# Optimization experiments

Hardware: AMD Instinct MI355X
Metric: run time of the kernel (lower is better)

The kernel has to match this reference:

```python
import jax, jax.numpy as jnp
import numpy as np

K = 3
STRIDE = 1
PAD = 1
DIL = 1


def conv2d(x, w, b, stride, pad, dil):
    y = jax.lax.conv_general_dilated(
        x, w, (stride, stride), [(pad, pad), (pad, pad)],
        rhs_dilation=(dil, dil), dimension_numbers=("NCHW", "OIHW", "NCHW"))
    return y + b[None, :, None, None]


def bilinear_gather(img, ys, xs):
    # img: (C,H,W); ys,xs: (KK,Ho,Wo) pixel coords.
    # grid_sample(mode=bilinear, padding_mode=zeros, align_corners=True):
    # out-of-range corners contribute 0, interpolation weights unchanged.
    H, W = img.shape[-2:]
    y0 = jnp.floor(ys)
    x0 = jnp.floor(xs)
    wy1 = ys - y0
    wx1 = xs - x0
    wy0 = 1.0 - wy1
    wx0 = 1.0 - wx1

    def g(yc, xc):
        yi = yc.astype(jnp.int32)
        xi = xc.astype(jnp.int32)
        valid = (yi >= 0) & (yi < H) & (xi >= 0) & (xi < W)
        yi = jnp.clip(yi, 0, H - 1)
        xi = jnp.clip(xi, 0, W - 1)
        v = img[:, yi, xi]  # (C,KK,Ho,Wo)
        return v * valid[None].astype(img.dtype)

    return (g(y0, x0) * (wy0 * wx0)[None]
            + g(y0, x0 + 1.0) * (wy0 * wx1)[None]
            + g(y0 + 1.0, x0) * (wy1 * wx0)[None]
            + g(y0 + 1.0, x0 + 1.0) * (wy1 * wx1)[None])


def setup_inputs() -> dict:
    key = jax.random.key(0)
    ks = jax.random.split(key, 4)
    B, C_in, H, W = 8, 64, 96, 96
    C_out = 64
    x = jax.random.normal(ks[0], (B, C_in, H, W), dtype=jnp.float32)
    weight = jax.random.normal(ks[1], (C_out, C_in, K, K), dtype=jnp.float32) * 0.05
    bias = jax.random.normal(ks[2], (C_out,), dtype=jnp.float32) * 0.01
    off_w = jax.random.normal(ks[3], (2 * K * K, C_in, K, K), dtype=jnp.float32) * 0.05
    off_b = jnp.zeros((2 * K * K,), dtype=jnp.float32)
    return {"x": x, "weight": weight, "bias": bias, "off_w": off_w, "off_b": off_b}


def reference(x, weight, bias, off_w, off_b):
    B, C, H, W = x.shape
    Ho = (H + 2 * PAD - DIL * (K - 1) - 1) // STRIDE + 1
    Wo = (W + 2 * PAD - DIL * (K - 1) - 1) // STRIDE + 1

    offsets = conv2d(x, off_w, off_b, STRIDE, PAD, DIL)  # (B,2*K*K,Ho,Wo)
    off = offsets.reshape(B, K * K, 2, Ho, Wo)

    # Base sampling grid (note: original code does NOT subtract padding; kept faithful).
    by, bx = jnp.meshgrid(jnp.arange(Ho, dtype=x.dtype), jnp.arange(Wo, dtype=x.dtype), indexing="ij")
    by = by * STRIDE + (K // 2) * DIL
    bx = bx * STRIDE + (K // 2) * DIL
    ko = jnp.arange(-(K // 2), K // 2 + 1, dtype=x.dtype)
    ky, kx = jnp.meshgrid(ko, ko, indexing="ij")

    sy = by[None, None] + ky.reshape(1, -1, 1, 1) + off[:, :, 0]  # (B,KK,Ho,Wo)
    sx = bx[None, None] + kx.reshape(1, -1, 1, 1) + off[:, :, 1]

    sampled = jax.vmap(bilinear_gather)(x, sy, sx)  # (B,C,KK,Ho,Wo)

    wflat = weight.reshape(weight.shape[0], C, K * K)  # (O,C,KK)
    out = jnp.einsum("bckhw,ock->bohw", sampled, wflat)
    return out + bias[None, :, None, None]
```

## Files before the change

### kernel.cpp

```cpp
#include <hip/hip_runtime.h>
#include <hip/hip_bf16.h>

#define HH 96
#define WW 96
#define HW 9216
#define NB 8

typedef __bf16 bf16x8 __attribute__((ext_vector_type(8)));
typedef float  f32x4  __attribute__((ext_vector_type(4)));

union BF8 { uint4 u; bf16x8 v; unsigned short s[8]; };

__device__ __forceinline__ unsigned short f2bf_bits(float f) {
    unsigned u = __float_as_uint(f);
    unsigned r = u + 0x7FFFu + ((u >> 16) & 1u);
    return (unsigned short)(r >> 16);
}
__device__ __forceinline__ float bf2f(unsigned short s) {
    return __uint_as_float(((unsigned)s) << 16);
}
__device__ __forceinline__ unsigned pkbf(float a, float b) {
    union { __hip_bfloat162 h; unsigned u; } c;
    c.h = __float22bfloat162_rn(make_float2(a, b));
    return c.u;
}

__device__ __forceinline__ void bl_setup(int h, int w, int r, int s, float oy, float ox,
                                         int* a, float* wg) {
    float sy = (float)(h + r) + oy;
    float sx = (float)(w + s) + ox;
    float fy = floorf(sy), fx = floorf(sx);
    int   y0 = (int)fy, x0 = (int)fx;
    int   y1 = y0 + 1, x1 = x0 + 1;
    float wy1 = sy - fy, wx1 = sx - fx;
    float wy0 = 1.f - wy1, wx0 = 1.f - wx1;
    float m00 = (y0 >= 0 && y0 < HH && x0 >= 0 && x0 < WW) ? 1.f : 0.f;
    float m01 = (y0 >= 0 && y0 < HH && x1 >= 0 && x1 < WW) ? 1.f : 0.f;
    float m10 = (y1 >= 0 && y1 < HH && x0 >= 0 && x0 < WW) ? 1.f : 0.f;
    float m11 = (y1 >= 0 && y1 < HH && x1 >= 0 && x1 < WW) ? 1.f : 0.f;
    int cy0 = min(max(y0, 0), HH - 1), cy1 = min(max(y1, 0), HH - 1);
    int cx0 = min(max(x0, 0), WW - 1), cx1 = min(max(x1, 0), WW - 1);
    a[0] = (cy0 * WW + cx0) * 64;  a[1] = (cy0 * WW + cx1) * 64;
    a[2] = (cy1 * WW + cx0) * 64;  a[3] = (cy1 * WW + cx1) * 64;
    wg[0] = wy0 * wx0 * m00;  wg[1] = wy0 * wx1 * m01;
    wg[2] = wy1 * wx0 * m10;  wg[3] = wy1 * wx1 * m11;
}

__global__ __launch_bounds__(256) void xcvt_prep(const float* __restrict__ x,
                                                 const float* __restrict__ weight,
                                                 const float* __restrict__ off_w,
                                                 unsigned short* __restrict__ xt,
                                                 unsigned short* __restrict__ wTb,
                                                 unsigned short* __restrict__ owTb) {
    __shared__ unsigned short T[64 * 64];
    int bid   = blockIdx.x;
    int t     = threadIdx.x;
    int b     = bid & 7;
    int pbase = (bid >> 3) * 64;
    int pl    = t & 63;
    int q     = t >> 6;

    const float* xp = x + ((size_t)(b * 64 + q * 16)) * HW + pbase + pl;
    unsigned short hb[16];
#pragma unroll
    for (int i = 0; i < 16; ++i) hb[i] = f2bf_bits(xp[(size_t)i * HW]);

    uint4 w0, w1;
    w0.x = hb[0]  | (hb[1]  << 16); w0.y = hb[2]  | (hb[3]  << 16);
    w0.z = hb[4]  | (hb[5]  << 16); w0.w = hb[6]  | (hb[7]  << 16);
    w1.x = hb[8]  | (hb[9]  << 16); w1.y = hb[10] | (hb[11] << 16);
    w1.z = hb[12] | (hb[13] << 16); w1.w = hb[14] | (hb[15] << 16);
    int sw = pl & 7;
    *(uint4*)&T[pl * 64 + (((2 * q)     ^ sw) << 3)] = w0;
    *(uint4*)&T[pl * 64 + (((2 * q + 1) ^ sw) << 3)] = w1;
    __syncthreads();

    int row = t >> 2, rs = row & 7;
    uint4 a  = *(const uint4*)&T[row * 64 + ((((t & 3) * 2)     ^ rs) << 3)];
    uint4 b2 = *(const uint4*)&T[row * 64 + ((((t & 3) * 2 + 1) ^ rs) << 3)];
    unsigned short* dst = xt + ((size_t)(b * HW + pbase)) * 64 + t * 16;
    *(uint4*)dst       = a;
    *(uint4*)(dst + 8) = b2;

    if (bid < 216) {
        int i = bid * 256 + t;
        if (i < 36864) {
            int tap = i >> 12;
            int co  = (i >> 6) & 63;
            int c   = i & 63;
            wTb[i] = f2bf_bits(weight[(co * 64 + c) * 9 + tap]);
        } else {
            int f   = i - 36864;
            int j   = f / 576;
            int kk  = f - j * 576;
            int tap = kk >> 6;
            int c   = kk & 63;
            owTb[f] = (j < 18) ? f2bf_bits(off_w[(j * 64 + c) * 9 + tap]) : (unsigned short)0;
        }
    }
}

__global__ __launch_bounds__(256) void deform_all(const unsigned short* __restrict__ xt,
                                                  const unsigned short* __restrict__ wTb,
                                                  const unsigned short* __restrict__ owTb,
                                                  const float* __restrict__ bias,
                                                  const float* __restrict__ ob,
                                                  float* __restrict__ out) {
    __shared__ unsigned short S[2][32 * 64];
    __shared__ float offs[32 * 20];

    int bid   = blockIdx.x;
    int t     = threadIdx.x;
    int b     = bid & 7;
    int pbase = (bid >> 3) * 32;

    int e   = t & 7;
    int pxl = t >> 3;
    int px  = pbase + pxl;
    int h   = px / WW, w = px - h * WW;
    int sw  = pxl & 7;

    int ln = t & 15;
    int qd = (t >> 4) & 3;
    int wv = t >> 6;

    const unsigned short* xb = xt + (size_t)b * HW * 64;

    int ptA = wv & 1, jtA = wv >> 1;
    f32x4 accj = {0.f, 0.f, 0.f, 0.f};

    for (int tap = 0; tap < 9; ++tap) {
        int cur = tap & 1;
        int r = tap / 3, s = tap - r * 3;

        int  iy = h - 1 + r, ix = w - 1 + s;
        bool vd = (iy >= 0) & (iy < HH) & (ix >= 0) & (ix < WW);
        int  ad = (min(max(iy, 0), HH - 1) * WW + min(max(ix, 0), WW - 1)) * 64;
        uint4 p = *(const uint4*)(xb + ad + e * 8);
        if (!vd) p = make_uint4(0, 0, 0, 0);
        *(uint4*)&S[cur][pxl * 64 + ((e ^ sw) << 3)] = p;
        __syncthreads();

        int  row = ptA * 16 + ln, rs = row & 7;
        BF8  fa0, fa1, fb0, fb1;
        fa0.u = *(const uint4*)&S[cur][row * 64 + ((qd       ^ rs) << 3)];
        fa1.u = *(const uint4*)&S[cur][row * 64 + (((qd + 4) ^ rs) << 3)];
        const unsigned short* brow = owTb + (size_t)(jtA * 16 + ln) * 576 + tap * 64 + qd * 8;
        fb0.u = *(const uint4*)brow;
        fb1.u = *(const uint4*)(brow + 32);
        accj = __builtin_amdgcn_mfma_f32_16x16x32_bf16(fa0.v, fb0.v, accj, 0, 0, 0);
        accj = __builtin_amdgcn_mfma_f32_16x16x32_bf16(fa1.v, fb1.v, accj, 0, 0, 0);
    }

    {
        int j = jtA * 16 + ln;
        if (j < 18) {
            int   rowp = ptA * 16 + qd * 4;
            float obj  = ob[j];
#pragma unroll
            for (int rg = 0; rg < 4; ++rg) offs[(rowp + rg) * 20 + j] = accj[rg] + obj;
        }
    }
    __syncthreads();

    float oy[9], ox[9];
#pragma unroll
    for (int k = 0; k < 9; ++k) {
        float2 p = *(const float2*)&offs[pxl * 20 + 2 * k];
        oy[k] = p.x; ox[k] = p.y;
    }

    f32x4 acc[2] = {{0.f,0.f,0.f,0.f},{0.f,0.f,0.f,0.f}};

    for (int tap = 0; tap < 9; ++tap) {
        int cur = tap & 1;
        int r = tap / 3, s = tap - r * 3;

        int   a[4];
        float g[4];
        bl_setup(h, w, r, s, oy[tap], ox[tap], a, g);

        uint4 cA[4];
#pragma unroll
        for (int c = 0; c < 4; ++c) cA[c] = *(const uint4*)(xb + a[c] + e * 8);

        BF8 q0, q1, q2, q3;
        q0.u = cA[0]; q1.u = cA[1]; q2.u = cA[2]; q3.u = cA[3];
        float v[8];
#pragma unroll
        for (int i = 0; i < 8; ++i)
            v[i] = g[0] * bf2f(q0.s[i]) + g[1] * bf2f(q1.s[i])
                 + g[2] * bf2f(q2.s[i]) + g[3] * bf2f(q3.s[i]);
        uint4 sv;
        sv.x = pkbf(v[0], v[1]); sv.y = pkbf(v[2], v[3]);
        sv.z = pkbf(v[4], v[5]); sv.w = pkbf(v[6], v[7]);
        *(uint4*)&S[cur][pxl * 64 + ((e ^ sw) << 3)] = sv;
        __syncthreads();

        {
            const unsigned short* wb = wTb + (size_t)tap * 4096 + (wv * 16 + ln) * 64 + qd * 8;
            BF8 fb0, fb1;
            fb0.u = *(const uint4*)wb;
            fb1.u = *(const uint4*)(wb + 32);
#pragma unroll
            for (int pt = 0; pt < 2; ++pt) {
                int row = pt * 16 + ln, rs = row & 7;
                BF8 fa0, fa1;
                fa0.u = *(const uint4*)&S[cur][row * 64 + ((qd       ^ rs) << 3)];
                fa1.u = *(const uint4*)&S[cur][row * 64 + (((qd + 4) ^ rs) << 3)];
                acc[pt] = __builtin_amdgcn_mfma_f32_16x16x32_bf16(fa0.v, fb0.v, acc[pt], 0, 0, 0);
                acc[pt] = __builtin_amdgcn_mfma_f32_16x16x32_bf16(fa1.v, fb1.v, acc[pt], 0, 0, 0);
            }
        }
    }

    int   co = wv * 16 + ln;
    float bv = bias[co];
    float* ob2 = out + ((size_t)(b * 64 + co)) * HW + pbase + qd * 4;
#pragma unroll
    for (int pt = 0; pt < 2; ++pt) {
        float4 st;
        st.x = acc[pt].x + bv; st.y = acc[pt].y + bv;
        st.z = acc[pt].z + bv; st.w = acc[pt].w + bv;
        *(float4*)(ob2 + pt * 16) = st;
    }
}

extern "C" void kernel_launch(void* const* d_in, const int* in_sizes, int n_in,
                              void* d_out, int out_size, void* d_ws, size_t ws_size,
                              hipStream_t stream) {
    const float* x      = (const float*)d_in[0];
    const float* weight = (const float*)d_in[1];
    const float* bias   = (const float*)d_in[2];
    const float* off_w  = (const float*)d_in[3];
    const float* off_b  = (const float*)d_in[4];
    float* out = (float*)d_out;

    unsigned short* xt   = (unsigned short*)d_ws;
    unsigned short* wTb  = xt + 4718592;
    unsigned short* owTb = wTb + 36864;

    hipLaunchKernelGGL(xcvt_prep,  dim3(1152), dim3(256), 0, stream,
                       x, weight, off_w, xt, wTb, owTb);
    hipLaunchKernelGGL(deform_all, dim3(2304), dim3(256), 0, stream,
                       xt, wTb, owTb, bias, off_b, out);
}
```

Before: 136.1 us.

## Stage 3-row halo in LDS for offset conv and software-pipeline bilinear gathers

The offset-conv phase now loads a 3x34-pixel halo tile into shared memory once, then reads all 9 taps from it. This replaces a global load and barrier per tap. The deformable phase processes two taps per barrier step and issues the gathers for the next two taps before computing the current ones, to hide global latency. Launch bounds request 3 blocks per SM. The change assumes each 32-pixel block lies within one image row (96 is divisible by 32), and it raises register pressure from the prefetched gather buffers.

```diff
diff --git a/kernel.cpp b/kernel.cpp
--- a/kernel.cpp
+++ b/kernel.cpp
@@ -100,24 +100,25 @@
     }
 }
 
-__global__ __launch_bounds__(256) void deform_all(const unsigned short* __restrict__ xt,
-                                                  const unsigned short* __restrict__ wTb,
-                                                  const unsigned short* __restrict__ owTb,
-                                                  const float* __restrict__ bias,
-                                                  const float* __restrict__ ob,
-                                                  float* __restrict__ out) {
-    __shared__ unsigned short S[2][32 * 64];
+__global__ __launch_bounds__(256, 3) void deform_all(const unsigned short* __restrict__ xt,
+                                                     const unsigned short* __restrict__ wTb,
+                                                     const unsigned short* __restrict__ owTb,
+                                                     const float* __restrict__ bias,
+                                                     const float* __restrict__ ob,
+                                                     float* __restrict__ out) {
+    __shared__ unsigned short SH[2 * 2 * 32 * 64];
     __shared__ float offs[32 * 20];
 
     int bid   = blockIdx.x;
     int t     = threadIdx.x;
     int b     = bid & 7;
     int pbase = (bid >> 3) * 32;
+    int r0    = pbase / WW;
+    int c0    = pbase - r0 * WW;
 
     int e   = t & 7;
     int pxl = t >> 3;
-    int px  = pbase + pxl;
-    int h   = px / WW, w = px - h * WW;
+    int h   = r0, w = c0 + pxl;
     int sw  = pxl & 7;
 
     int ln = t & 15;
@@ -126,32 +127,36 @@
 
     const unsigned short* xb = xt + (size_t)b * HW * 64;
 
+#pragma unroll
+    for (int p = 0; p < 4; ++p) {
+        int rec = p * 32 + pxl;
+        if (rec < 102) {
+            int hr = rec / 34, hc = rec - hr * 34;
+            int gr = r0 - 1 + hr, gc = c0 - 1 + hc;
+            bool vd = (gr >= 0) & (gr < HH) & (gc >= 0) & (gc < WW);
+            uint4 v = make_uint4(0u, 0u, 0u, 0u);
+            if (vd) v = *(const uint4*)(xb + (size_t)(gr * WW + gc) * 64 + e * 8);
+            *(uint4*)&SH[rec * 64 + ((e ^ (hc & 7)) << 3)] = v;
+        }
+    }
+    __syncthreads();
+
     int ptA = wv & 1, jtA = wv >> 1;
     f32x4 accj = {0.f, 0.f, 0.f, 0.f};
-
+#pragma unroll
     for (int tap = 0; tap < 9; ++tap) {
-        int cur = tap & 1;
         int r = tap / 3, s = tap - r * 3;
-
-        int  iy = h - 1 + r, ix = w - 1 + s;
-        bool vd = (iy >= 0) & (iy < HH) & (ix >= 0) & (ix < WW);
-        int  ad = (min(max(iy, 0), HH - 1) * WW + min(max(ix, 0), WW - 1)) * 64;
-        uint4 p = *(const uint4*)(xb + ad + e * 8);
-        if (!vd) p = make_uint4(0, 0, 0, 0);
-        *(uint4*)&S[cur][pxl * 64 + ((e ^ sw) << 3)] = p;
-        __syncthreads();
-
-        int  row = ptA * 16 + ln, rs = row & 7;
-        BF8  fa0, fa1, fb0, fb1;
-        fa0.u = *(const uint4*)&S[cur][row * 64 + ((qd       ^ rs) << 3)];
-        fa1.u = *(const uint4*)&S[cur][row * 64 + (((qd + 4) ^ rs) << 3)];
+        int cH = ptA * 16 + ln + s;
+        int ba = (r * 34 + cH) * 64;
+        BF8 fa0, fa1, fb0, fb1;
+        fa0.u = *(const uint4*)&SH[ba + ((qd       ^ (cH & 7)) << 3)];
+        fa1.u = *(const uint4*)&SH[ba + (((qd + 4) ^ (cH & 7)) << 3)];
         const unsigned short* brow = owTb + (size_t)(jtA * 16 + ln) * 576 + tap * 64 + qd * 8;
         fb0.u = *(const uint4*)brow;
         fb1.u = *(const uint4*)(brow + 32);
         accj = __builtin_amdgcn_mfma_f32_16x16x32_bf16(fa0.v, fb0.v, accj, 0, 0, 0);
         accj = __builtin_amdgcn_mfma_f32_16x16x32_bf16(fa1.v, fb1.v, accj, 0, 0, 0);
     }
-
     {
         int j = jtA * 16 + ln;
         if (j < 18) {
@@ -172,46 +177,70 @@
 
     f32x4 acc[2] = {{0.f,0.f,0.f,0.f},{0.f,0.f,0.f,0.f}};
 
-    for (int tap = 0; tap < 9; ++tap) {
-        int cur = tap & 1;
+    uint4 cc[2][4], cn[2][4];
+    float gc[2][4], gn[2][4];
+
+    auto issue = [&](int tap, uint4 (&C)[4], float (&G)[4]) {
         int r = tap / 3, s = tap - r * 3;
-
-        int   a[4];
-        float g[4];
-        bl_setup(h, w, r, s, oy[tap], ox[tap], a, g);
-
-        uint4 cA[4];
-#pragma unroll
-        for (int c = 0; c < 4; ++c) cA[c] = *(const uint4*)(xb + a[c] + e * 8);
-
-        BF8 q0, q1, q2, q3;
-        q0.u = cA[0]; q1.u = cA[1]; q2.u = cA[2]; q3.u = cA[3];
-        float v[8];
-#pragma unroll
-        for (int i = 0; i < 8; ++i)
-            v[i] = g[0] * bf2f(q0.s[i]) + g[1] * bf2f(q1.s[i])
-                 + g[2] * bf2f(q2.s[i]) + g[3] * bf2f(q3.s[i]);
-        uint4 sv;
-        sv.x = pkbf(v[0], v[1]); sv.y = pkbf(v[2], v[3]);
-        sv.z = pkbf(v[4], v[5]); sv.w = pkbf(v[6], v[7]);
-        *(uint4*)&S[cur][pxl * 64 + ((e ^ sw) << 3)] = sv;
+        int aa[4];
+        bl_setup(h, w, r, s, oy[tap], ox[tap], aa, G);
+#pragma unroll
+        for (int c = 0; c < 4; ++c) C[c] = *(const uint4*)(xb + aa[c] + e * 8);
+    };
+
+    issue(0, cc[0], gc[0]);
+    issue(1, cc[1], gc[1]);
+
+#pragma unroll
+    for (int step = 0; step < 5; ++step) {
+        int  buf  = step & 1;
+        int  t0   = 2 * step;
+        bool has1 = (t0 + 1) < 9;
+
+        if (t0 + 2 < 9) issue(t0 + 2, cn[0], gn[0]);
+        if (t0 + 3 < 9) issue(t0 + 3, cn[1], gn[1]);
+
+#pragma unroll
+        for (int tp = 0; tp < 2; ++tp) {
+            if (tp == 0 || has1) {
+                BF8 q0, q1, q2, q3;
+                q0.u = cc[tp][0]; q1.u = cc[tp][1]; q2.u = cc[tp][2]; q3.u = cc[tp][3];
+                float vv[8];
+#pragma unroll
+                for (int i = 0; i < 8; ++i)
+                    vv[i] = gc[tp][0] * bf2f(q0.s[i]) + gc[tp][1] * bf2f(q1.s[i])
+                          + gc[tp][2] * bf2f(q2.s[i]) + gc[tp][3] * bf2f(q3.s[i]);
+                uint4 sv;
+                sv.x = pkbf(vv[0], vv[1]); sv.y = pkbf(vv[2], vv[3]);
+                sv.z = pkbf(vv[4], vv[5]); sv.w = pkbf(vv[6], vv[7]);
+                *(uint4*)&SH[((buf * 2 + tp) * 32 + pxl) * 64 + ((e ^ sw) << 3)] = sv;
+            }
+        }
         __syncthreads();
 
-        {
-            const unsigned short* wb = wTb + (size_t)tap * 4096 + (wv * 16 + ln) * 64 + qd * 8;
-            BF8 fb0, fb1;
-            fb0.u = *(const uint4*)wb;
-            fb1.u = *(const uint4*)(wb + 32);
-#pragma unroll
-            for (int pt = 0; pt < 2; ++pt) {
-                int row = pt * 16 + ln, rs = row & 7;
-                BF8 fa0, fa1;
-                fa0.u = *(const uint4*)&S[cur][row * 64 + ((qd       ^ rs) << 3)];
-                fa1.u = *(const uint4*)&S[cur][row * 64 + (((qd + 4) ^ rs) << 3)];
-                acc[pt] = __builtin_amdgcn_mfma_f32_16x16x32_bf16(fa0.v, fb0.v, acc[pt], 0, 0, 0);
-                acc[pt] = __builtin_amdgcn_mfma_f32_16x16x32_bf16(fa1.v, fb1.v, acc[pt], 0, 0, 0);
+#pragma unroll
+        for (int tp = 0; tp < 2; ++tp) {
+            if (tp == 0 || has1) {
+                int tk = t0 + tp;
+                const unsigned short* wb = wTb + (size_t)tk * 4096 + (wv * 16 + ln) * 64 + qd * 8;
+                BF8 fb0, fb1;
+                fb0.u = *(const uint4*)wb;
+                fb1.u = *(const uint4*)(wb + 32);
+#pragma unroll
+                for (int pt = 0; pt < 2; ++pt) {
+                    int row = pt * 16 + ln, rs2 = row & 7;
+                    BF8 fa0, fa1;
+                    fa0.u = *(const uint4*)&SH[((buf * 2 + tp) * 32 + row) * 64 + ((qd       ^ rs2) << 3)];
+                    fa1.u = *(const uint4*)&SH[((buf * 2 + tp) * 32 + row) * 64 + (((qd + 4) ^ rs2) << 3)];
+                    acc[pt] = __builtin_amdgcn_mfma_f32_16x16x32_bf16(fa0.v, fb0.v, acc[pt], 0, 0, 0);
+                    acc[pt] = __builtin_amdgcn_mfma_f32_16x16x32_bf16(fa1.v, fb1.v, acc[pt], 0, 0, 0);
+                }
             }
         }
+#pragma unroll
+        for (int tp = 0; tp < 2; ++tp)
+#pragma unroll
+            for (int c = 0; c < 4; ++c) { cc[tp][c] = cn[tp][c]; gc[tp][c] = gn[tp][c]; }
     }
 
     int   co = wv * 16 + ln;
```

After: 131.4 us, median of 2. 1.04x faster.
